# Optimization experiments

Hardware: AMD Instinct MI355X
Metric: run time of the kernel (lower is better)

Reference implementation:

```python
import jax, jax.numpy as jnp
import numpy as np

N, M, C, MID, K = 131072, 4096, 32, 16, 6
BN_EPS = 1e-5


def _bn(x, g, b, mu, var):
    # eval-mode BatchNorm over channel (last) axis
    return g * (x - mu) * jax.lax.rsqrt(var + BN_EPS) + b


def _block(x, w1, b1, g, b, mu, var, w2, b2):
    # Conv1d(kernel_size=1) stack == per-position linear over channels
    h = jax.nn.relu(_bn(x @ w1.T + b1, g, b, mu, var))
    return h @ w2.T + b2


def _l2norm(x):
    # F.normalize(p=2, dim=channel) with eps=1e-12 clamp
    return x / jnp.maximum(jnp.linalg.norm(x, axis=-1, keepdims=True), 1e-12)


def _forward(sp_fea, sp_xyz, o_p_fea, p_xyz, idx_abs, idx_rel, params):
    (wf1_w, wf1_b, wf_g, wf_b, wf_m, wf_v, wf2_w, wf2_b,
     wx1_w, wx1_b, wx_g, wx_b, wx_m, wx_v, wx2_w, wx2_b,
     m1_w, m1_b, mb_g, mb_b, mb_m, mb_v, m2_w, m2_b) = params
    m = sp_fea.shape[1]
    c = o_p_fea.shape[1]
    # gather each point's K candidate superpoint fea/xyz, center on the point
    c2p_fea = sp_fea[0][idx_abs] - o_p_fea[:, None, :]   # (n, K, C)
    c2p_xyz = sp_xyz[0][idx_abs] - p_xyz[:, None, :]     # (n, K, 3)
    # point MLP: Linear -> BN -> ReLU -> Linear
    p_fea = jax.nn.relu(_bn(o_p_fea @ m1_w.T + m1_b, mb_g, mb_b, mb_m, mb_v)) @ m2_w.T + m2_b  # (n, C)
    w_fea = _block(c2p_fea, wf1_w, wf1_b, wf_g, wf_b, wf_m, wf_v, wf2_w, wf2_b)  # (n, K, C)
    w_xyz = _block(c2p_xyz, wx1_w, wx1_b, wx_g, wx_b, wx_m, wx_v, wx2_w, wx2_b)  # (n, K, C)
    p_fea, w_fea, w_xyz = _l2norm(p_fea), _l2norm(w_fea), _l2norm(w_xyz)
    # bilateral weights over the K candidates
    bi_w = jax.nn.softmax(
        jnp.einsum('nc,nkc->nk', p_fea, w_fea) * jnp.einsum('nc,nkc->nk', p_fea, w_xyz),
        axis=-1)  # (n, K)
    # weighted segment aggregation points -> superpoints
    # (equivalent to building the dense (m, n) association matrix f and matmul)
    ridx = idx_rel.reshape(-1)                                     # (n*K,)
    wsum = jax.ops.segment_sum(bi_w.reshape(-1), ridx, num_segments=m)  # (m,)
    agg_fea = jax.ops.segment_sum((bi_w[..., None] * o_p_fea[:, None, :]).reshape(-1, c), ridx, num_segments=m)
    agg_xyz = jax.ops.segment_sum((bi_w[..., None] * p_xyz[:, None, :]).reshape(-1, 3), ridx, num_segments=m)
    denom = wsum[:, None] + 1e-8
    return (agg_fea / denom)[None], (agg_xyz / denom)[None]  # (1, m, C), (1, m, 3)


def setup_inputs() -> dict:
    key = jax.random.key(0)
    ks = jax.random.split(key, 20)
    f32 = jnp.float32
    idx = jax.random.randint(ks[4], (1, N, K), 0, M, dtype=jnp.int32)
    inp = {
        'sp_fea': jax.random.normal(ks[0], (1, M, C), f32),
        'sp_xyz': jax.random.normal(ks[1], (1, M, 3), f32),
        'o_p_fea': jax.random.normal(ks[2], (N, C), f32),
        'p_xyz': jax.random.normal(ks[3], (N, 3), f32),
        'c2p_idx_abs': idx,
        'c2p_idx': idx,  # bs=1 -> absolute == relative indices
        'cluster_idx': jax.random.randint(ks[5], (N,), 0, M, dtype=jnp.int32),
        'offset': jnp.array([N], dtype=jnp.int32),
        'wf1_w': jax.random.normal(ks[6], (MID, C), f32) * 0.2,
        'wf1_b': jnp.zeros((MID,), f32),
        'wf_bn_g': jnp.ones((MID,), f32),
        'wf_bn_b': jnp.zeros((MID,), f32),
        'wf_bn_m': jax.random.normal(ks[7], (MID,), f32) * 0.1,
        'wf_bn_v': jax.random.uniform(ks[8], (MID,), f32, 0.5, 1.5),
        'wf2_w': jax.random.normal(ks[9], (C, MID), f32) * 0.2,
        'wf2_b': jnp.zeros((C,), f32),
        'wx1_w': jax.random.normal(ks[10], (MID, 3), f32) * 0.2,
        'wx1_b': jnp.zeros((MID,), f32),
        'wx_bn_g': jnp.ones((MID,), f32),
        'wx_bn_b': jnp.zeros((MID,), f32),
        'wx_bn_m': jax.random.normal(ks[11], (MID,), f32) * 0.1,
        'wx_bn_v': jax.random.uniform(ks[12], (MID,), f32, 0.5, 1.5),
        'wx2_w': jax.random.normal(ks[13], (C, MID), f32) * 0.2,
        'wx2_b': jnp.zeros((C,), f32),
        'mlp1_w': jax.random.normal(ks[14], (C, C), f32) * 0.2,
        'mlp1_b': jnp.zeros((C,), f32),
        'mlp_bn_g': jnp.ones((C,), f32),
        'mlp_bn_b': jnp.zeros((C,), f32),
        'mlp_bn_m': jax.random.normal(ks[15], (C,), f32) * 0.1,
        'mlp_bn_v': jax.random.uniform(ks[16], (C,), f32, 0.5, 1.5),
        'mlp2_w': jax.random.normal(ks[17], (C, C), f32) * 0.2,
        'mlp2_b': jnp.zeros((C,), f32),
    }
    return inp


def reference(sp_fea, sp_xyz, o_p_fea, p_xyz, c2p_idx_abs, c2p_idx, cluster_idx, offset,
              wf1_w, wf1_b, wf_bn_g, wf_bn_b, wf_bn_m, wf_bn_v, wf2_w, wf2_b,
              wx1_w, wx1_b, wx_bn_g, wx_bn_b, wx_bn_m, wx_bn_v, wx2_w, wx2_b,
              mlp1_w, mlp1_b, mlp_bn_g, mlp_bn_b, mlp_bn_m, mlp_bn_v, mlp2_w, mlp2_b):
    params = (wf1_w, wf1_b, wf_bn_g, wf_bn_b, wf_bn_m, wf_bn_v, wf2_w, wf2_b,
              wx1_w, wx1_b, wx_bn_g, wx_bn_b, wx_bn_m, wx_bn_v, wx2_w, wx2_b,
              mlp1_w, mlp1_b, mlp_bn_g, mlp_bn_b, mlp_bn_m, mlp_bn_v, mlp2_w, mlp2_b)
    return _forward(sp_fea, sp_xyz, o_p_fea, p_xyz, c2p_idx_abs[0], c2p_idx[0], params)
```

## Files before the change

kernel.cpp:

```cpp
#include <hip/hip_runtime.h>

#define M_ 4096
#define N_ 131072
#define K_ 6
#define C_ 32
#define MID_ 16
#define CAP_ 320
#define CNT_STRIDE 16
#define PB 32
#define PKS 68

#define OFF_AF 0
#define OFF_AX (M_*MID_)
#define OFF_CB (2*M_*MID_)
#define CB_WF1T 0
#define CB_WX1T 512
#define CB_M1T  576
#define CB_TM   1600
#define CB_QFMT 1632
#define CB_QXMT 2144
#define CB_QF0  2656
#define CB_QX0  2672
#define CB_G2   2688
#define CB_M2TB 3712
#define CB_PBFV 3744
#define CB_PBXV 3776
#define CB_UF   3808
#define CB_UX   4064
#define CB_CF   4320
#define CB_CX   4336
#define CB_SC   4352
#define CB_N    4360
#define OFF_CNT  (OFF_CB + CB_N + 8)
#define OFF_PAIR (OFF_CNT + M_*CNT_STRIDE)

#define BN_EPS 1e-5f

__global__ void prep_kernel(
    const float* __restrict__ sp_fea, const float* __restrict__ sp_xyz,
    const float* __restrict__ wf1_w, const float* __restrict__ wf1_b,
    const float* __restrict__ wf_g, const float* __restrict__ wf_b,
    const float* __restrict__ wf_m, const float* __restrict__ wf_v,
    const float* __restrict__ wf2_w, const float* __restrict__ wf2_b,
    const float* __restrict__ wx1_w, const float* __restrict__ wx1_b,
    const float* __restrict__ wx_g, const float* __restrict__ wx_b,
    const float* __restrict__ wx_m, const float* __restrict__ wx_v,
    const float* __restrict__ wx2_w, const float* __restrict__ wx2_b,
    const float* __restrict__ m1_w, const float* __restrict__ m1_b,
    const float* __restrict__ mb_g, const float* __restrict__ mb_b,
    const float* __restrict__ mb_m, const float* __restrict__ mb_v,
    const float* __restrict__ m2_w, const float* __restrict__ m2_b,
    float* __restrict__ ws)
{
    const int gid = blockIdx.x * blockDim.x + threadIdx.x;

    if (gid < M_) {
        float sp[32];
        #pragma unroll
        for (int q = 0; q < 8; ++q) {
            float4 v = *(const float4*)(sp_fea + gid*32 + 4*q);
            sp[4*q] = v.x; sp[4*q+1] = v.y; sp[4*q+2] = v.z; sp[4*q+3] = v.w;
        }
        #pragma unroll
        for (int j = 0; j < 16; ++j) {
            float s = wf_g[j] * rsqrtf(wf_v[j] + BN_EPS);
            float t = s * wf1_b[j] + wf_b[j] - s * wf_m[j];
            float acc = 0.f;
            #pragma unroll
            for (int c = 0; c < 32; ++c) acc += sp[c] * wf1_w[j*32 + c];
            ws[OFF_AF + gid*16 + j] = s * acc + t;
        }
        float sx0 = sp_xyz[gid*3], sx1 = sp_xyz[gid*3+1], sx2 = sp_xyz[gid*3+2];
        #pragma unroll
        for (int j = 0; j < 16; ++j) {
            float s = wx_g[j] * rsqrtf(wx_v[j] + BN_EPS);
            float t = s * wx1_b[j] + wx_b[j] - s * wx_m[j];
            float acc = sx0*wx1_w[j*3] + sx1*wx1_w[j*3+1] + sx2*wx1_w[j*3+2];
            ws[OFF_AX + gid*16 + j] = s * acc + t;
        }
    }

    if (blockIdx.x == 0) {
        __shared__ float sG[512];
        __shared__ float svv[40];
        const int t = threadIdx.x;
        float* cb = ws + OFF_CB;

        for (int e = t; e < 512; e += 256) {
            int c = e >> 4, jj = e & 15;
            float s = wf_g[jj] * rsqrtf(wf_v[jj] + BN_EPS);
            cb[CB_WF1T + e] = s * wf1_w[jj*32 + c];
            float aqf = 0.f, aqx = 0.f;
            #pragma unroll
            for (int i = 0; i < 32; ++i) {
                aqf += wf2_w[i*16 + jj] * m2_w[i*32 + c];
                aqx += wx2_w[i*16 + jj] * m2_w[i*32 + c];
            }
            cb[CB_QFMT + e] = aqf;
            cb[CB_QXMT + e] = aqx;
        }
        if (t < 64) {
            int c = t >> 4, jj = t & 15;
            float s = wx_g[jj] * rsqrtf(wx_v[jj] + BN_EPS);
            cb[CB_WX1T + t] = (c < 3) ? s * wx1_w[jj*3 + c] : 0.f;
        }
        for (int e = t; e < 1024; e += 256) {
            int c = e >> 5, i = e & 31;
            float s = mb_g[i] * rsqrtf(mb_v[i] + BN_EPS);
            cb[CB_M1T + e] = s * m1_w[i*32 + c];
            int q = e >> 5, p = e & 31;
            float a = 0.f;
            #pragma unroll
            for (int i2 = 0; i2 < 32; ++i2) a += m2_w[i2*32 + q] * m2_w[i2*32 + p];
            cb[CB_G2 + e] = a;
        }
        if (t < 32) {
            float s = mb_g[t] * rsqrtf(mb_v[t] + BN_EPS);
            cb[CB_TM + t] = s * m1_b[t] + mb_b[t] - s * mb_m[t];
            float a = 0.f, bf = 0.f, bx = 0.f;
            #pragma unroll
            for (int i2 = 0; i2 < 32; ++i2) {
                a  += m2_w[i2*32 + t] * m2_b[i2];
                bf += m2_w[i2*32 + t] * wf2_b[i2];
                bx += m2_w[i2*32 + t] * wx2_b[i2];
            }
            cb[CB_M2TB + t] = a;
            cb[CB_PBFV + t] = bf;
            cb[CB_PBXV + t] = bx;
        }
        {
            int jj = t >> 4, p = t & 15;
            float accf = 0.f, accx = 0.f;
            #pragma unroll
            for (int i2 = 0; i2 < 32; ++i2) {
                accf += wf2_w[i2*16 + jj] * wf2_w[i2*16 + p];
                accx += wx2_w[i2*16 + jj] * wx2_w[i2*16 + p];
            }
            sG[t]       = accf;
            sG[256 + t] = accx;
        }
        if (t < 16) {
            float q0f = 0.f, q0x = 0.f, vf = 0.f, vx = 0.f;
            #pragma unroll
            for (int i2 = 0; i2 < 32; ++i2) {
                q0f += wf2_w[i2*16 + t] * m2_b[i2];
                q0x += wx2_w[i2*16 + t] * m2_b[i2];
                vf  += wf2_w[i2*16 + t] * wf2_b[i2];
                vx  += wx2_w[i2*16 + t] * wx2_b[i2];
            }
            cb[CB_QF0 + t] = q0f;
            cb[CB_QX0 + t] = q0x;
            svv[t]      = vf;
            svv[16 + t] = vx;
        }
        if (t == 0) {
            float bbf = 0.f, bbx = 0.f, bb2 = 0.f, pcf = 0.f, pcx = 0.f;
            #pragma unroll
            for (int i2 = 0; i2 < 32; ++i2) {
                bbf += wf2_b[i2]*wf2_b[i2];
                bbx += wx2_b[i2]*wx2_b[i2];
                bb2 += m2_b[i2]*m2_b[i2];
                pcf += m2_b[i2]*wf2_b[i2];
                pcx += m2_b[i2]*wx2_b[i2];
            }
            svv[32] = bbf; svv[33] = bbx;
            cb[CB_SC+2] = bb2;
            cb[CB_SC+3] = pcf; cb[CB_SC+4] = pcx;
            cb[CB_SC+5] = 0.f; cb[CB_SC+6] = 0.f; cb[CB_SC+7] = 0.f;
        }
        __syncthreads();

        if (t < 64) {
            const int lane = t;
            const int half = lane >> 5;
            const int p    = lane & 31;
            const bool act = (p < 16);
            const int pp   = p & 15;
            const int sb   = half ? 32 : 0;

            float c[16];
            #pragma unroll
            for (int k = 0; k < 16; ++k)
                c[k] = act ? sG[half*256 + k*16 + pp] : 0.f;

            float u[16];
            #pragma unroll
            for (int k = 0; k < 16; ++k) {
                const float gkk = __shfl(c[k], sb + k);
                const float d = sqrtf(fmaxf(gkk, 1e-30f));
                const float ukp = c[k] / d;
                u[k] = ukp;
                #pragma unroll
                for (int j2 = k + 1; j2 < 16; ++j2)
                    c[j2] -= __shfl(ukp, sb + j2) * ukp;
            }

            const float v = act ? svv[half*16 + pp] : 0.f;
            float acc = 0.f, cf = 0.f;
            #pragma unroll
            for (int i = 0; i < 16; ++i) {
                const float cand = (v - acc) / u[i];
                const float ci = __shfl(cand, sb + i);
                if (pp == i) cf = ci;
                acc += ((i <= pp) ? u[i] : 0.f) * ci;
            }
            float s2 = act ? cf * cf : 0.f;
            s2 += __shfl_xor(s2, 1); s2 += __shfl_xor(s2, 2);
            s2 += __shfl_xor(s2, 4); s2 += __shfl_xor(s2, 8);

            if (act) {
                float* dst = ws + OFF_CB + (half ? CB_UX : CB_UF);
                #pragma unroll
                for (int k = 0; k < 16; ++k)
                    dst[k*16 + pp] = (k <= pp) ? u[k] : 0.f;
                ws[OFF_CB + (half ? CB_CX : CB_CF) + pp] = cf;
                if (pp == 0) ws[OFF_CB + CB_SC + half] = svv[32 + half] - s2;
            }
        }
    }
}

__global__ __launch_bounds__(256) void fused_kernel(
    const float* __restrict__ o_p_fea, const float* __restrict__ p_xyz,
    const int* __restrict__ idx_abs, float* __restrict__ ws)
{
    __shared__ float cb[CB_N];
    __shared__ float ovl[PB*33 + PB*36];
    float* opl = ovl;
    float* hpb = ovl + PB*33;
    float* pkl = ovl;

    const int tid = threadIdx.x;
    const int base = blockIdx.x * PB;
    {
        const float* src = ws + OFF_CB;
        for (int i = tid; i < CB_N; i += 256) cb[i] = src[i];
        #pragma unroll
        for (int u = 0; u < 4; ++u) {
            const int idx = tid + u*256;
            opl[(idx >> 5)*33 + (idx & 31)] = o_p_fea[(size_t)base*32 + idx];
        }
    }
    __syncthreads();

    const int g = tid >> 4;
    const int j = tid & 15;
    const int n0 = base + 2*g;
    const int n1 = n0 + 1;

    float af0=0.f, af1=0.f, h00=0.f, h01=0.f, h10=0.f, h11=0.f;
    #pragma unroll
    for (int c = 0; c < 32; ++c) {
        const float op0 = opl[(2*g)*33 + c];
        const float op1 = opl[(2*g+1)*33 + c];
        const float w   = cb[CB_WF1T + c*16 + j];
        const float m0  = cb[CB_M1T + c*32 + 2*j];
        const float m1v = cb[CB_M1T + c*32 + 2*j + 1];
        af0 += w*op0;  af1 += w*op1;
        h00 += m0*op0; h01 += m1v*op0;
        h10 += m0*op1; h11 += m1v*op1;
    }
    {
        const float tm0 = cb[CB_TM + 2*j], tm1 = cb[CB_TM + 2*j + 1];
        h00 = fmaxf(h00 + tm0, 0.f); h01 = fmaxf(h01 + tm1, 0.f);
        h10 = fmaxf(h10 + tm0, 0.f); h11 = fmaxf(h11 + tm1, 0.f);
    }
    const float wx0 = cb[CB_WX1T + j], wx1v = cb[CB_WX1T + 16 + j], wx2v = cb[CB_WX1T + 32 + j];
    const float ax0 = wx0*p_xyz[n0*3] + wx1v*p_xyz[n0*3+1] + wx2v*p_xyz[n0*3+2];
    const float ax1 = wx0*p_xyz[n1*3] + wx1v*p_xyz[n1*3+1] + wx2v*p_xyz[n1*3+2];

    hpb[(2*g)*36 + 2*j]       = h00;
    hpb[(2*g)*36 + 2*j + 1]   = h01;
    hpb[(2*g+1)*36 + 2*j]     = h10;
    hpb[(2*g+1)*36 + 2*j + 1] = h11;
    __syncthreads();

    const float q0i = cb[CB_QF0 + j], qx0i = cb[CB_QX0 + j];
    float qf0 = q0i, qf1 = q0i, qx0 = qx0i, qx1 = qx0i;
    float t200=0.f, t201=0.f, t210=0.f, t211=0.f;
    #pragma unroll
    for (int q = 0; q < 32; ++q) {
        const float hq0 = hpb[(2*g)*36 + q];
        const float hq1 = hpb[(2*g+1)*36 + q];
        const float wqf = cb[CB_QFMT + q*16 + j];
        const float wqx = cb[CB_QXMT + q*16 + j];
        const float ga  = cb[CB_G2 + q*32 + 2*j];
        const float gb  = cb[CB_G2 + q*32 + 2*j + 1];
        qf0 += wqf*hq0; qf1 += wqf*hq1;
        qx0 += wqx*hq0; qx1 += wqx*hq1;
        t200 += ga*hq0; t201 += gb*hq0;
        t210 += ga*hq1; t211 += gb*hq1;
    }
    const float m2tb0 = 2.f*cb[CB_M2TB + 2*j], m2tb1 = 2.f*cb[CB_M2TB + 2*j + 1];
    const float pbv0 = cb[CB_PBFV + 2*j], pbv1 = cb[CB_PBFV + 2*j + 1];
    const float pxv0 = cb[CB_PBXV + 2*j], pxv1 = cb[CB_PBXV + 2*j + 1];
    float pn20 = h00*(t200 + m2tb0) + h01*(t201 + m2tb1);
    float pn21 = h10*(t210 + m2tb0) + h11*(t211 + m2tb1);
    float pbf0 = h00*pbv0 + h01*pbv1;
    float pbf1 = h10*pbv0 + h11*pbv1;
    float pbx0 = h00*pxv0 + h01*pxv1;
    float pbx1 = h10*pxv0 + h11*pxv1;
    #pragma unroll
    for (int mm = 1; mm < 16; mm <<= 1) {
        pn20 += __shfl_xor(pn20, mm, 16);
        pn21 += __shfl_xor(pn21, mm, 16);
        pbf0 += __shfl_xor(pbf0, mm, 16);
        pbf1 += __shfl_xor(pbf1, mm, 16);
        pbx0 += __shfl_xor(pbx0, mm, 16);
        pbx1 += __shfl_xor(pbx1, mm, 16);
    }
    const float sc2v = cb[CB_SC + 2], sc3v = cb[CB_SC + 3], sc4v = cb[CB_SC + 4];
    const float inv0 = 1.0f / fmaxf(sqrtf(fmaxf(pn20 + sc2v, 0.f)), 1e-12f);
    const float inv1 = 1.0f / fmaxf(sqrtf(fmaxf(pn21 + sc2v, 0.f)), 1e-12f);

    __syncthreads();

    ((float4*)(pkl + (2*g)*PKS))[j]   = make_float4(af0, ax0, qf0*inv0, qx0*inv0);
    ((float4*)(pkl + (2*g+1)*PKS))[j] = make_float4(af1, ax1, qf1*inv1, qx1*inv1);
    if (j == 0) {
        pkl[(2*g)*PKS + 64]   = (pbf0 + sc3v) * inv0;
        pkl[(2*g)*PKS + 65]   = (pbx0 + sc4v) * inv0;
        pkl[(2*g+1)*PKS + 64] = (pbf1 + sc3v) * inv1;
        pkl[(2*g+1)*PKS + 65] = (pbx1 + sc4v) * inv1;
    }
    __syncthreads();

    const int slot = tid >> 3;
    const int k    = tid & 7;
    const int n    = base + slot;
    const int kc   = (k < K_) ? k : (K_ - 1);
    const int r    = idx_abs[n * K_ + kc];
    const float* pkb = pkl + slot*PKS;

    float afr[16], axr[16];
    #pragma unroll
    for (int q4 = 0; q4 < 4; ++q4) {
        float4 a = *(const float4*)(ws + OFF_AF + r*16 + 4*q4);
        float4 b = *(const float4*)(ws + OFF_AX + r*16 + 4*q4);
        afr[4*q4] = a.x; afr[4*q4+1] = a.y; afr[4*q4+2] = a.z; afr[4*q4+3] = a.w;
        axr[4*q4] = b.x; axr[4*q4+1] = b.y; axr[4*q4+2] = b.z; axr[4*q4+3] = b.w;
    }

    float hf[16], hx[16];
    float df = 0.f, dx = 0.f;
    #pragma unroll
    for (int jj = 0; jj < 16; ++jj) {
        const float4 v4 = ((const float4*)pkb)[jj];
        const float h1 = fmaxf(afr[jj] - v4.x, 0.f);
        const float h2 = fmaxf(axr[jj] - v4.y, 0.f);
        hf[jj] = h1; hx[jj] = h2;
        df += v4.z * h1;
        dx += v4.w * h2;
    }
    const float scbx = pkb[64], scby = pkb[65];

    float nf = cb[CB_SC + 0], nx = cb[CB_SC + 1];
    #pragma unroll
    for (int q = 0; q < 16; ++q) {
        float yf = cb[CB_CF + q];
        float yx = cb[CB_CX + q];
        #pragma unroll
        for (int p4 = (q >> 2); p4 < 4; ++p4) {
            const float4 uf = *(const float4*)&cb[CB_UF + q*16 + 4*p4];
            const float4 ux = *(const float4*)&cb[CB_UX + q*16 + 4*p4];
            yf += uf.x*hf[4*p4] + uf.y*hf[4*p4+1] + uf.z*hf[4*p4+2] + uf.w*hf[4*p4+3];
            yx += ux.x*hx[4*p4] + ux.y*hx[4*p4+1] + ux.z*hx[4*p4+2] + ux.w*hx[4*p4+3];
        }
        nf += yf * yf;
        nx += yx * yx;
    }
    const float invf = 1.0f / fmaxf(sqrtf(fmaxf(nf, 0.f)), 1e-12f);
    const float invx = 1.0f / fmaxf(sqrtf(fmaxf(nx, 0.f)), 1e-12f);
    float logit = ((df + scbx) * invf) * ((dx + scby) * invx);
    if (k >= K_) logit = -3.0e38f;

    float mx = logit;
    mx = fmaxf(mx, __shfl_xor(mx, 1));
    mx = fmaxf(mx, __shfl_xor(mx, 2));
    mx = fmaxf(mx, __shfl_xor(mx, 4));
    float ex = __expf(logit - mx);
    float s = ex;
    s += __shfl_xor(s, 1);
    s += __shfl_xor(s, 2);
    s += __shfl_xor(s, 4);
    const float w = ex / s;

    if (k < K_) {
        int*  cnt   = (int*)(ws + OFF_CNT);
        int2* pairs = (int2*)(ws + OFF_PAIR);
        const int pos = atomicAdd(&cnt[r*CNT_STRIDE], 1);
        if (pos < CAP_) {
            pairs[(size_t)r*CAP_ + pos] = make_int2(n, __float_as_int(w));
        }
    }
}

__global__ __launch_bounds__(256) void agg_kernel(
    const float* __restrict__ ws,
    const float* __restrict__ o_p_fea, const float* __restrict__ p_xyz,
    float* __restrict__ out)
{
    __shared__ float red[4][40];

    const int wave = threadIdx.x >> 6;
    const int lane = threadIdx.x & 63;
    const int m = blockIdx.x;
    const int eo = lane >> 5;
    const int c  = lane & 31;

    const int*  cnt   = (const int*)(ws + OFF_CNT);
    const int2* pairs = (const int2*)(ws + OFF_PAIR);

    int cn = cnt[m*CNT_STRIDE];
    if (cn > CAP_) cn = CAP_;
    const int2* pb = pairs + (size_t)m * CAP_;

    float acc = 0.f, wacc = 0.f, xacc = 0.f;
    for (int e2 = (wave*2 + eo)*2; e2 < cn; e2 += 16) {
        const int4 pq = *(const int4*)&pb[e2];
        {
            const int nn  = pq.x;
            const float w = __int_as_float(pq.y);
            acc += w * o_p_fea[(size_t)nn*32 + c];
            if (c == 0) wacc += w;
            if (c < 3)  xacc += w * p_xyz[nn*3 + c];
        }
        if (e2 + 1 < cn) {
            const int nn  = pq.z;
            const float w = __int_as_float(pq.w);
            acc += w * o_p_fea[(size_t)nn*32 + c];
            if (c == 0) wacc += w;
            if (c < 3)  xacc += w * p_xyz[nn*3 + c];
        }
    }
    acc  += __shfl_xor(acc, 32);
    xacc += __shfl_xor(xacc, 32);
    wacc += __shfl_xor(wacc, 32);
    if (eo == 0) {
        red[wave][c] = acc;
        if (c < 3)  red[wave][33 + c] = xacc;
        if (c == 0) red[wave][36] = wacc;
    }
    __syncthreads();

    if (wave == 0 && eo == 0) {
        const float a = red[0][c] + red[1][c] + red[2][c] + red[3][c];
        const float wtot = red[0][36] + red[1][36] + red[2][36] + red[3][36];
        const float denom = wtot + 1e-8f;
        out[m*32 + c] = a / denom;
        if (c < 3) {
            const float x = red[0][33+c] + red[1][33+c] + red[2][33+c] + red[3][33+c];
            out[M_*C_ + m*3 + c] = x / denom;
        }
    }
}

extern "C" void kernel_launch(void* const* d_in, const int* in_sizes, int n_in,
                              void* d_out, int out_size, void* d_ws, size_t ws_size,
                              hipStream_t stream)
{
    const float* sp_fea  = (const float*)d_in[0];
    const float* sp_xyz  = (const float*)d_in[1];
    const float* o_p_fea = (const float*)d_in[2];
    const float* p_xyz   = (const float*)d_in[3];
    const int*   idx_abs = (const int*)d_in[4];
    const float* wf1_w = (const float*)d_in[8];
    const float* wf1_b = (const float*)d_in[9];
    const float* wf_g  = (const float*)d_in[10];
    const float* wf_b  = (const float*)d_in[11];
    const float* wf_m  = (const float*)d_in[12];
    const float* wf_v  = (const float*)d_in[13];
    const float* wf2_w = (const float*)d_in[14];
    const float* wf2_b = (const float*)d_in[15];
    const float* wx1_w = (const float*)d_in[16];
    const float* wx1_b = (const float*)d_in[17];
    const float* wx_g  = (const float*)d_in[18];
    const float* wx_b  = (const float*)d_in[19];
    const float* wx_m  = (const float*)d_in[20];
    const float* wx_v  = (const float*)d_in[21];
    const float* wx2_w = (const float*)d_in[22];
    const float* wx2_b = (const float*)d_in[23];
    const float* m1_w  = (const float*)d_in[24];
    const float* m1_b  = (const float*)d_in[25];
    const float* mb_g  = (const float*)d_in[26];
    const float* mb_b  = (const float*)d_in[27];
    const float* mb_m  = (const float*)d_in[28];
    const float* mb_v  = (const float*)d_in[29];
    const float* m2_w  = (const float*)d_in[30];
    const float* m2_b  = (const float*)d_in[31];

    float* ws = (float*)d_ws;
    float* out = (float*)d_out;

    hipMemsetAsync(ws + OFF_CNT, 0, (size_t)(M_*CNT_STRIDE) * sizeof(int), stream);

    prep_kernel<<<16, 256, 0, stream>>>(
        sp_fea, sp_xyz,
        wf1_w, wf1_b, wf_g, wf_b, wf_m, wf_v, wf2_w, wf2_b,
        wx1_w, wx1_b, wx_g, wx_b, wx_m, wx_v, wx2_w, wx2_b,
        m1_w, m1_b, mb_g, mb_b, mb_m, mb_v, m2_w, m2_b,
        ws);

    fused_kernel<<<N_/PB, 256, 0, stream>>>(o_p_fea, p_xyz, idx_abs, ws);

    agg_kernel<<<M_, 256, 0, stream>>>(ws, o_p_fea, p_xyz, out);
}
```

Measured before the change: 132.7 us.

## Make fused kernel wave-private per 8 points with wave barriers

Each 64-lane wave now owns 8 points and a private shared-memory region, so the block-wide __syncthreads between the point-MLP stages and the candidate stage become wave-level barriers. The o_p_fea tile load is vectorised to float4 per wave, and the idx_abs gather is hoisted before the first barrier to overlap its latency. This removes cross-wave stalls but depends on correct LDS waitcnt ordering inside the wave.

```diff
diff --git a/kernel.cpp b/kernel.cpp
--- a/kernel.cpp
+++ b/kernel.cpp
@@ -8,6 +8,7 @@
 #define CAP_ 320
 #define CNT_STRIDE 16
 #define PB 32
+#define WCH 576
 #define PKS 68
 
 #define OFF_AF 0
@@ -225,40 +226,50 @@
     const int* __restrict__ idx_abs, float* __restrict__ ws)
 {
     __shared__ float cb[CB_N];
-    __shared__ float ovl[PB*33 + PB*36];
-    float* opl = ovl;
-    float* hpb = ovl + PB*33;
-    float* pkl = ovl;
-
-    const int tid = threadIdx.x;
-    const int base = blockIdx.x * PB;
+    __shared__ float ovl[4*WCH];
+
+    const int tid  = threadIdx.x;
+    const int w    = tid >> 6;
+    const int lane = tid & 63;
+    const int base = blockIdx.x * PB + w*8;
+    float* wb = ovl + w*WCH;
+    float* hpw = wb + 288;
+
     {
         const float* src = ws + OFF_CB;
         for (int i = tid; i < CB_N; i += 256) cb[i] = src[i];
-        #pragma unroll
-        for (int u = 0; u < 4; ++u) {
-            const int idx = tid + u*256;
-            opl[(idx >> 5)*33 + (idx & 31)] = o_p_fea[(size_t)base*32 + idx];
-        }
-    }
+        const int row  = lane >> 3;
+        const int col4 = (lane & 7) << 2;
+        *(float4*)(wb + row*36 + col4) =
+            *(const float4*)(o_p_fea + (size_t)(base + row)*32 + col4);
+    }
+
+    const int slot = lane >> 3;
+    const int k    = lane & 7;
+    const int nB   = base + slot;
+    const int kc   = (k < K_) ? k : (K_ - 1);
+    const int r    = idx_abs[nB * K_ + kc];
+
     __syncthreads();
 
-    const int g = tid >> 4;
-    const int j = tid & 15;
-    const int n0 = base + 2*g;
+    const int gl = lane >> 4;
+    const int j  = lane & 15;
+    const int n0 = base + 2*gl;
     const int n1 = n0 + 1;
+    const float* opl0 = wb + (2*gl)*36;
+    const float* opl1 = opl0 + 36;
 
     float af0=0.f, af1=0.f, h00=0.f, h01=0.f, h10=0.f, h11=0.f;
     #pragma unroll
     for (int c = 0; c < 32; ++c) {
-        const float op0 = opl[(2*g)*33 + c];
-        const float op1 = opl[(2*g+1)*33 + c];
-        const float w   = cb[CB_WF1T + c*16 + j];
+        const float op0 = opl0[c];
+        const float op1 = opl1[c];
+        const float wv  = cb[CB_WF1T + c*16 + j];
         const float m0  = cb[CB_M1T + c*32 + 2*j];
         const float m1v = cb[CB_M1T + c*32 + 2*j + 1];
-        af0 += w*op0;  af1 += w*op1;
-        h00 += m0*op0; h01 += m1v*op0;
-        h10 += m0*op1; h11 += m1v*op1;
+        af0 += wv*op0;  af1 += wv*op1;
+        h00 += m0*op0;  h01 += m1v*op0;
+        h10 += m0*op1;  h11 += m1v*op1;
     }
     {
         const float tm0 = cb[CB_TM + 2*j], tm1 = cb[CB_TM + 2*j + 1];
@@ -269,19 +280,20 @@
     const float ax0 = wx0*p_xyz[n0*3] + wx1v*p_xyz[n0*3+1] + wx2v*p_xyz[n0*3+2];
     const float ax1 = wx0*p_xyz[n1*3] + wx1v*p_xyz[n1*3+1] + wx2v*p_xyz[n1*3+2];
 
-    hpb[(2*g)*36 + 2*j]       = h00;
-    hpb[(2*g)*36 + 2*j + 1]   = h01;
-    hpb[(2*g+1)*36 + 2*j]     = h10;
-    hpb[(2*g+1)*36 + 2*j + 1] = h11;
-    __syncthreads();
+    hpw[(2*gl)*36 + 2*j]       = h00;
+    hpw[(2*gl)*36 + 2*j + 1]   = h01;
+    hpw[(2*gl+1)*36 + 2*j]     = h10;
+    hpw[(2*gl+1)*36 + 2*j + 1] = h11;
+    asm volatile("s_waitcnt lgkmcnt(0)" ::: "memory");
+    __builtin_amdgcn_wave_barrier();
 
     const float q0i = cb[CB_QF0 + j], qx0i = cb[CB_QX0 + j];
     float qf0 = q0i, qf1 = q0i, qx0 = qx0i, qx1 = qx0i;
     float t200=0.f, t201=0.f, t210=0.f, t211=0.f;
     #pragma unroll
     for (int q = 0; q < 32; ++q) {
-        const float hq0 = hpb[(2*g)*36 + q];
-        const float hq1 = hpb[(2*g+1)*36 + q];
+        const float hq0 = hpw[(2*gl)*36 + q];
+        const float hq1 = hpw[(2*gl+1)*36 + q];
         const float wqf = cb[CB_QFMT + q*16 + j];
         const float wqx = cb[CB_QXMT + q*16 + j];
         const float ga  = cb[CB_G2 + q*32 + 2*j];
@@ -313,24 +325,20 @@
     const float inv0 = 1.0f / fmaxf(sqrtf(fmaxf(pn20 + sc2v, 0.f)), 1e-12f);
     const float inv1 = 1.0f / fmaxf(sqrtf(fmaxf(pn21 + sc2v, 0.f)), 1e-12f);
 
-    __syncthreads();
-
-    ((float4*)(pkl + (2*g)*PKS))[j]   = make_float4(af0, ax0, qf0*inv0, qx0*inv0);
-    ((float4*)(pkl + (2*g+1)*PKS))[j] = make_float4(af1, ax1, qf1*inv1, qx1*inv1);
+    __builtin_amdgcn_wave_barrier();
+
+    ((float4*)(wb + (2*gl)*PKS))[j]   = make_float4(af0, ax0, qf0*inv0, qx0*inv0);
+    ((float4*)(wb + (2*gl+1)*PKS))[j] = make_float4(af1, ax1, qf1*inv1, qx1*inv1);
     if (j == 0) {
-        pkl[(2*g)*PKS + 64]   = (pbf0 + sc3v) * inv0;
-        pkl[(2*g)*PKS + 65]   = (pbx0 + sc4v) * inv0;
-        pkl[(2*g+1)*PKS + 64] = (pbf1 + sc3v) * inv1;
-        pkl[(2*g+1)*PKS + 65] = (pbx1 + sc4v) * inv1;
-    }
-    __syncthreads();
-
-    const int slot = tid >> 3;
-    const int k    = tid & 7;
-    const int n    = base + slot;
-    const int kc   = (k < K_) ? k : (K_ - 1);
-    const int r    = idx_abs[n * K_ + kc];
-    const float* pkb = pkl + slot*PKS;
+        wb[(2*gl)*PKS + 64]   = (pbf0 + sc3v) * inv0;
+        wb[(2*gl)*PKS + 65]   = (pbx0 + sc4v) * inv0;
+        wb[(2*gl+1)*PKS + 64] = (pbf1 + sc3v) * inv1;
+        wb[(2*gl+1)*PKS + 65] = (pbx1 + sc4v) * inv1;
+    }
+    asm volatile("s_waitcnt lgkmcnt(0)" ::: "memory");
+    __builtin_amdgcn_wave_barrier();
+
+    const float* pkb = wb + slot*PKS;
 
     float afr[16], axr[16];
     #pragma unroll
@@ -383,14 +391,14 @@
     s += __shfl_xor(s, 1);
     s += __shfl_xor(s, 2);
     s += __shfl_xor(s, 4);
-    const float w = ex / s;
+    const float w2 = ex / s;
 
     if (k < K_) {
         int*  cnt   = (int*)(ws + OFF_CNT);
         int2* pairs = (int2*)(ws + OFF_PAIR);
         const int pos = atomicAdd(&cnt[r*CNT_STRIDE], 1);
         if (pos < CAP_) {
-            pairs[(size_t)r*CAP_ + pos] = make_int2(n, __float_as_int(w));
+            pairs[(size_t)r*CAP_ + pos] = make_int2(nB, __float_as_int(w2));
         }
     }
 }
```

New measurement: 141.9 us. +7.0%, slower.

## Fold counter zeroing into prep kernel and stage pair lists in LDS for aggregation

Applied to the files above, without the earlier changes.

The separate memset of the per-superpoint counters is removed and the zeroing is done inside prep_kernel, which saves one launch. The aggregation kernel now copies each superpoint's (index, weight) pair list into shared memory and gives each half-wave a contiguous chunk. The chunk is processed four entries at a time so several independent gathers are in flight together. This adds a block-wide barrier and shared-memory use in exchange for better latency hiding and fewer dependent global loads.

```diff
diff --git a/kernel.cpp b/kernel.cpp
--- a/kernel.cpp
+++ b/kernel.cpp
@@ -55,6 +55,12 @@
     const int gid = blockIdx.x * blockDim.x + threadIdx.x;
 
     if (gid < M_) {
+        int4* cz = (int4*)((int*)(ws + OFF_CNT) + gid*CNT_STRIDE);
+        const int4 z = make_int4(0, 0, 0, 0);
+        cz[0] = z; cz[1] = z; cz[2] = z; cz[3] = z;
+    }
+
+    if (gid < M_) {
         float sp[32];
         #pragma unroll
         for (int q = 0; q < 8; ++q) {
@@ -400,13 +406,16 @@
     const float* __restrict__ o_p_fea, const float* __restrict__ p_xyz,
     float* __restrict__ out)
 {
+    __shared__ int2 pl[CAP_];
     __shared__ float red[4][40];
 
-    const int wave = threadIdx.x >> 6;
-    const int lane = threadIdx.x & 63;
+    const int tid  = threadIdx.x;
+    const int wave = tid >> 6;
+    const int lane = tid & 63;
     const int m = blockIdx.x;
     const int eo = lane >> 5;
     const int c  = lane & 31;
+    const int hw = wave*2 + eo;
 
     const int*  cnt   = (const int*)(ws + OFF_CNT);
     const int2* pairs = (const int2*)(ws + OFF_PAIR);
@@ -415,24 +424,36 @@
     if (cn > CAP_) cn = CAP_;
     const int2* pb = pairs + (size_t)m * CAP_;
 
+    for (int i = tid; i < cn; i += 256) pl[i] = pb[i];
+    __syncthreads();
+
+    const int chunk = (cn + 7) >> 3;
+    const int s0   = hw * chunk;
+    const int epos = min(s0 + chunk, cn);
+
     float acc = 0.f, wacc = 0.f, xacc = 0.f;
-    for (int e2 = (wave*2 + eo)*2; e2 < cn; e2 += 16) {
-        const int4 pq = *(const int4*)&pb[e2];
-        {
-            const int nn  = pq.x;
-            const float w = __int_as_float(pq.y);
-            acc += w * o_p_fea[(size_t)nn*32 + c];
-            if (c == 0) wacc += w;
-            if (c < 3)  xacc += w * p_xyz[nn*3 + c];
-        }
-        if (e2 + 1 < cn) {
-            const int nn  = pq.z;
-            const float w = __int_as_float(pq.w);
-            acc += w * o_p_fea[(size_t)nn*32 + c];
-            if (c == 0) wacc += w;
-            if (c < 3)  xacc += w * p_xyz[nn*3 + c];
-        }
-    }
+    for (int e = s0; e < epos; e += 4) {
+        int   nn[4];
+        float wv[4];
+        #pragma unroll
+        for (int u = 0; u < 4; ++u) {
+            if (e + u < epos) {
+                const int2 p = pl[e + u];
+                nn[u] = p.x;
+                wv[u] = __int_as_float(p.y);
+            } else {
+                nn[u] = 0;
+                wv[u] = 0.f;
+            }
+        }
+        #pragma unroll
+        for (int u = 0; u < 4; ++u) {
+            acc += wv[u] * o_p_fea[(size_t)nn[u]*32 + c];
+            if (c == 0) wacc += wv[u];
+            if (c < 3)  xacc += wv[u] * p_xyz[nn[u]*3 + c];
+        }
+    }
+
     acc  += __shfl_xor(acc, 32);
     xacc += __shfl_xor(xacc, 32);
     wacc += __shfl_xor(wacc, 32);
@@ -492,8 +513,6 @@
     float* ws = (float*)d_ws;
     float* out = (float*)d_out;
 
-    hipMemsetAsync(ws + OFF_CNT, 0, (size_t)(M_*CNT_STRIDE) * sizeof(int), stream);
-
     prep_kernel<<<16, 256, 0, stream>>>(
         sp_fea, sp_xyz,
         wf1_w, wf1_b, wf_g, wf_b, wf_m, wf_v, wf2_w, wf2_b,
```

After: 120.6 us. -9.1%, faster.
